# Performance work log

Hardware: AMD Instinct MI355X
Metric: run time of the kernel (lower is better)

## Reference

```python
import jax, jax.numpy as jnp
import numpy as np

B, LQ, LK = 8, 512, 512
DQ = DK = DV = 512
H = 128


def setup_inputs() -> dict:
    key = jax.random.key(0)
    kq, kk, kv, k1, k2, k3 = jax.random.split(key, 6)
    query = jax.random.normal(kq, (B, LQ, DQ), dtype=jnp.float32)
    key_t = jax.random.normal(kk, (B, LK, DK), dtype=jnp.float32)
    value = jax.random.normal(kv, (B, LK, DV), dtype=jnp.float32)
    # Linear weights stored torch-style as (out_features, in_features)
    w1 = jax.random.normal(k1, (H, DQ), dtype=jnp.float32) / np.sqrt(DQ)
    w2 = jax.random.normal(k2, (H, DK), dtype=jnp.float32) / np.sqrt(DK)
    v = jax.random.normal(k3, (1, H), dtype=jnp.float32) / np.sqrt(H)
    return {"query": query, "key": key_t, "value": value, "w1": w1, "w2": w2, "v": v}


def reference(query, key, value, w1, w2, v):
    # Linear projections first (mathematically identical to projecting the
    # broadcast tensors, since Linear is linear): (B,Lq,H), (B,Lk,H)
    q_proj = jnp.einsum("bqd,hd->bqh", query, w1)
    k_proj = jnp.einsum("bkd,hd->bkh", key, w2)
    # Broadcast add -> tanh -> project to scalar: (B,Lq,Lk,H) intermediate
    feat = jnp.tanh(q_proj[:, :, None, :] + k_proj[:, None, :, :])
    score = jnp.einsum("bqkh,h->bqk", feat, v[0])
    attention_weights = jax.nn.softmax(score, axis=-1)
    context_vector = jnp.einsum("bqk,bkv->bqv", attention_weights, value)
    return (attention_weights, context_vector)
```

## Files before the change

kernel.cpp:

```cpp
#include <hip/hip_runtime.h>

#define TWO_LOG2E 2.8853900817779268f

__device__ __forceinline__ float frcp(float x) {
#if __has_builtin(__builtin_amdgcn_rcpf)
  return __builtin_amdgcn_rcpf(x);
#else
  return 1.0f / x;
#endif
}
__device__ __forceinline__ float fexp2(float x) {
#if __has_builtin(__builtin_amdgcn_exp2f)
  return __builtin_amdgcn_exp2f(x);
#else
  return exp2f(x);
#endif
}
__device__ __forceinline__ unsigned short f2bf(float f) {
  unsigned int u = __float_as_uint(f);
  u += 0x7fffu + ((u >> 16) & 1u);
  return (unsigned short)(u >> 16);
}
__device__ __forceinline__ unsigned int pack2bf(float lo, float hi) {
  return (unsigned int)f2bf(lo) | ((unsigned int)f2bf(hi) << 16);
}

using short8 = __attribute__((ext_vector_type(8))) short;
using f32x4v = __attribute__((ext_vector_type(4))) float;
using f32x8s = __attribute__((ext_vector_type(8))) float;
using f32x2 = __attribute__((ext_vector_type(2))) float;

__device__ __forceinline__ f32x2 pkfma(f32x2 a, f32x2 b, f32x2 c) {
  return __builtin_elementwise_fma(a, b, c);
}
__device__ __forceinline__ f32x2 splat2(float x) {
  f32x2 r;
  r.x = x;
  r.y = x;
  return r;
}
__device__ __forceinline__ f32x2 unpack_bf2(unsigned u) {
  f32x2 r;
  r.x = __uint_as_float(u << 16);
  r.y = __uint_as_float(u & 0xffff0000u);
  return r;
}
__device__ __forceinline__ void cell4k(float a0, float a1, float a2, float a3,
                                       f32x2 b0, f32x2 b1, f32x2 b2, f32x2 b3,
                                       float v0, float v1, float v2, float v3,
                                       f32x2& s) {
  const f32x2 one = {1.f, 1.f};
  f32x2 x0 = pkfma(splat2(a0), b0, one);
  f32x2 x1 = pkfma(splat2(a1), b1, one);
  f32x2 x2 = pkfma(splat2(a2), b2, one);
  f32x2 x3 = pkfma(splat2(a3), b3, one);
  f32x2 p01 = x0 * x1, p23 = x2 * x3;
  f32x2 n01 = pkfma(splat2(v0), x1, splat2(v1) * x0);
  f32x2 n23 = pkfma(splat2(v2), x3, splat2(v3) * x2);
  f32x2 num = pkfma(n01, p23, n23 * p01);
  f32x2 den = p01 * p23;
  f32x2 r;
  r.x = frcp(den.x);
  r.y = frcp(den.y);
  s = pkfma(num, r, s);
}

__global__ __launch_bounds__(256) void k_pre(
    const float* __restrict__ query, const float* __restrict__ key,
    const float* __restrict__ w1, const float* __restrict__ w2,
    const float* __restrict__ value,
    float* __restrict__ Aout, unsigned short* __restrict__ BoutT,
    unsigned short* __restrict__ valT) {
  __shared__ __align__(16) char Abuf[16 * 128];
  __shared__ __align__(16) char Bbuf[128 * 128];
  __shared__ unsigned short ts[64][66];

  const int t = threadIdx.x;

  if (blockIdx.y == 0) {
    const int px = blockIdx.x;
    const bool isB = px >= 256;
    const float* in = isB ? key : query;
    const float* wm = isB ? w2 : w1;
    const int m0g = (px & 255) * 16;
    const int w = t >> 6, l = t & 63;

    f32x4v acc[2];
    acc[0] = 0;
    acc[1] = 0;

    float4 aS;
    float4 wS[4][2];

#define P_LOAD(k0_)                                                        \
  {                                                                        \
    aS = *(const float4*)&in[(m0g + (t >> 4)) * 512 + (k0_) + (t & 15) * 4]; \
    _Pragma("unroll") for (int i = 0; i < 4; ++i) {                        \
      int tt = t + i * 256;                                                \
      int row = tt >> 3, g = tt & 7;                                       \
      const float* src = &wm[row * 512 + (k0_) + g * 8];                   \
      wS[i][0] = *(const float4*)src;                                      \
      wS[i][1] = *(const float4*)(src + 4);                                \
    }                                                                      \
  }
#define P_WRITE()                                                          \
  {                                                                        \
    int arow = t >> 4, q4 = t & 15;                                        \
    *(uint2*)(Abuf + arow * 128 + (((q4 >> 1) ^ (arow & 7)) << 4) +        \
              ((q4 & 1) << 3)) =                                           \
        make_uint2(pack2bf(aS.x, aS.y), pack2bf(aS.z, aS.w));              \
    _Pragma("unroll") for (int i = 0; i < 4; ++i) {                        \
      int tt = t + i * 256;                                                \
      int row = tt >> 3, g = tt & 7;                                       \
      uint4 p = make_uint4(                                                \
          pack2bf(wS[i][0].x, wS[i][0].y), pack2bf(wS[i][0].z, wS[i][0].w),\
          pack2bf(wS[i][1].x, wS[i][1].y), pack2bf(wS[i][1].z, wS[i][1].w));\
      *(uint4*)(Bbuf + row * 128 + ((g ^ (row & 7)) << 4)) = p;            \
    }                                                                      \
  }

    P_LOAD(0);
#pragma unroll
    for (int ks8 = 0; ks8 < 8; ++ks8) {
      if (ks8) __syncthreads();
      P_WRITE();
      if (ks8 < 7) P_LOAD(ks8 * 64 + 64);
      __syncthreads();
#pragma unroll
      for (int ks = 0; ks < 2; ++ks) {
        const int gb = ks * 4 + (l >> 4);
        const int ra = l & 15;
        short8 af = *(const short8*)(Abuf + ra * 128 + ((gb ^ (ra & 7)) << 4));
#pragma unroll
        for (int ni = 0; ni < 2; ++ni) {
          const int rb = w * 32 + ni * 16 + (l & 15);
          short8 bf_ = *(const short8*)(Bbuf + rb * 128 + ((gb ^ (rb & 7)) << 4));
          if (isB)
            acc[ni] = __builtin_amdgcn_mfma_f32_16x16x32_bf16(bf_, af, acc[ni], 0, 0, 0);
          else
            acc[ni] = __builtin_amdgcn_mfma_f32_16x16x32_bf16(af, bf_, acc[ni], 0, 0, 0);
        }
      }
    }
#undef P_LOAD
#undef P_WRITE
    if (!isB) {
#pragma unroll
      for (int ni = 0; ni < 2; ++ni) {
        int col = w * 32 + ni * 16 + (l & 15);
#pragma unroll
        for (int j = 0; j < 4; ++j) {
          int row = m0g + (l >> 4) * 4 + j;
          Aout[row * 128 + col] = fexp2(acc[ni][j] * TWO_LOG2E);
        }
      }
    } else {
      int m = m0g + (l & 15);
#pragma unroll
      for (int ni = 0; ni < 2; ++ni)
#pragma unroll
        for (int j = 0; j < 4; ++j) {
          int h = w * 32 + ni * 16 + (l >> 4) * 4 + j;
          BoutT[h * 4096 + m] = f2bf(fexp2(acc[ni][j] * TWO_LOG2E));
        }
    }
  } else {
    const int x = blockIdx.x;
    const int b = x >> 6, k0 = ((x >> 3) & 7) * 64, n0 = (x & 7) * 64;
    {
      int kr = t >> 4, n4 = (t & 15) * 4;
#pragma unroll
      for (int i = 0; i < 4; ++i) {
        float4 f =
            *(const float4*)&value[((b * 512) + k0 + kr + 16 * i) * 512 + n0 + n4];
        *(ushort4*)&ts[kr + 16 * i][n4] =
            make_ushort4(f2bf(f.x), f2bf(f.y), f2bf(f.z), f2bf(f.w));
      }
    }
    __syncthreads();
    {
      int nw = t >> 4, k4 = (t & 15) * 4;
#pragma unroll
      for (int i = 0; i < 4; ++i) {
        int n = nw + 16 * i;
        ushort4 o = make_ushort4(ts[k4 + 0][n], ts[k4 + 1][n], ts[k4 + 2][n],
                                 ts[k4 + 3][n]);
        *(ushort4*)&valT[((b * 512) + n0 + n) * 512 + k0 + k4] = o;
      }
    }
  }
}

__global__ __launch_bounds__(256, 4) void k_score_softmax(
    const float* __restrict__ Aexp, const unsigned short* __restrict__ BexpT,
    const float* __restrict__ vw, float* __restrict__ attn) {
  __shared__ float red[4][4];

  const int tid = threadIdx.x;
  const int b = blockIdx.y;
  const int qbase = blockIdx.x * 4;
  const int wav = tid >> 6;
  const int lane = tid & 63;

  const unsigned* const bbase32 = (const unsigned*)(BexpT + b * 512);
  const int kidx = wav * 64 + lane;

  const float* const pa0 =
      Aexp + __builtin_amdgcn_readfirstlane((b * 512 + qbase) * 128);
  const float* const pa1 = pa0 + 128;
  const float* const pa2 = pa0 + 256;
  const float* const pa3 = pa0 + 384;
  const float* const pv = vw;

  f32x2 acc0 = {0.f, 0.f}, acc1 = {0.f, 0.f};
  f32x2 acc2 = {0.f, 0.f}, acc3 = {0.f, 0.f};

#pragma unroll
  for (int ch = 0; ch < 16; ++ch) {
    f32x8s sa0, sa1, sa2, sa3, sv;
    unsigned soff = (unsigned)(ch * 32);
    asm volatile(
        "s_load_dwordx8 %0, %5, %10\n\t"
        "s_load_dwordx8 %1, %6, %10\n\t"
        "s_load_dwordx8 %2, %7, %10\n\t"
        "s_load_dwordx8 %3, %8, %10\n\t"
        "s_load_dwordx8 %4, %9, %10"
        : "=&s"(sa0), "=&s"(sa1), "=&s"(sa2), "=&s"(sa3), "=&s"(sv)
        : "s"(pa0), "s"(pa1), "s"(pa2), "s"(pa3), "s"(pv), "s"(soff));

    unsigned u[8];
#pragma unroll
    for (int j = 0; j < 8; ++j)
      u[j] = bbase32[ch * 16384 + j * 2048 + kidx];

    asm volatile("s_waitcnt lgkmcnt(0)"
                 : "+s"(sa0), "+s"(sa1), "+s"(sa2), "+s"(sa3), "+s"(sv));

#pragma unroll
    for (int g = 0; g < 2; ++g) {
      f32x2 b0 = unpack_bf2(u[g * 4 + 0]);
      f32x2 b1 = unpack_bf2(u[g * 4 + 1]);
      f32x2 b2 = unpack_bf2(u[g * 4 + 2]);
      f32x2 b3 = unpack_bf2(u[g * 4 + 3]);
      const int h = g * 4;
      cell4k(sa0[h], sa0[h + 1], sa0[h + 2], sa0[h + 3], b0, b1, b2, b3,
             sv[h], sv[h + 1], sv[h + 2], sv[h + 3], acc0);
      cell4k(sa1[h], sa1[h + 1], sa1[h + 2], sa1[h + 3], b0, b1, b2, b3,
             sv[h], sv[h + 1], sv[h + 2], sv[h + 3], acc1);
      cell4k(sa2[h], sa2[h + 1], sa2[h + 2], sa2[h + 3], b0, b1, b2, b3,
             sv[h], sv[h + 1], sv[h + 2], sv[h + 3], acc2);
      cell4k(sa3[h], sa3[h + 1], sa3[h + 2], sa3[h + 3], b0, b1, b2, b3,
             sv[h], sv[h + 1], sv[h + 2], sv[h + 3], acc3);
    }
  }

  float mn0 = fminf(acc0.x, acc0.y);
  float mn1 = fminf(acc1.x, acc1.y);
  float mn2 = fminf(acc2.x, acc2.y);
  float mn3 = fminf(acc3.x, acc3.y);
#pragma unroll
  for (int off = 32; off > 0; off >>= 1) {
    mn0 = fminf(mn0, __shfl_xor(mn0, off));
    mn1 = fminf(mn1, __shfl_xor(mn1, off));
    mn2 = fminf(mn2, __shfl_xor(mn2, off));
    mn3 = fminf(mn3, __shfl_xor(mn3, off));
  }
  if (lane == 0) {
    red[wav][0] = mn0; red[wav][1] = mn1; red[wav][2] = mn2; red[wav][3] = mn3;
  }
  __syncthreads();
  mn0 = fminf(fminf(red[0][0], red[1][0]), fminf(red[2][0], red[3][0]));
  mn1 = fminf(fminf(red[0][1], red[1][1]), fminf(red[2][1], red[3][1]));
  mn2 = fminf(fminf(red[0][2], red[1][2]), fminf(red[2][2], red[3][2]));
  mn3 = fminf(fminf(red[0][3], red[1][3]), fminf(red[2][3], red[3][3]));
  __syncthreads();

  float P0e = fexp2((mn0 - acc0.x) * TWO_LOG2E);
  float P0o = fexp2((mn0 - acc0.y) * TWO_LOG2E);
  float P1e = fexp2((mn1 - acc1.x) * TWO_LOG2E);
  float P1o = fexp2((mn1 - acc1.y) * TWO_LOG2E);
  float P2e = fexp2((mn2 - acc2.x) * TWO_LOG2E);
  float P2o = fexp2((mn2 - acc2.y) * TWO_LOG2E);
  float P3e = fexp2((mn3 - acc3.x) * TWO_LOG2E);
  float P3o = fexp2((mn3 - acc3.y) * TWO_LOG2E);
  float s0 = P0e + P0o, s1 = P1e + P1o, s2 = P2e + P2o, s3 = P3e + P3o;
#pragma unroll
  for (int off = 32; off > 0; off >>= 1) {
    s0 += __shfl_xor(s0, off);
    s1 += __shfl_xor(s1, off);
    s2 += __shfl_xor(s2, off);
    s3 += __shfl_xor(s3, off);
  }
  if (lane == 0) {
    red[wav][0] = s0; red[wav][1] = s1; red[wav][2] = s2; red[wav][3] = s3;
  }
  __syncthreads();
  float r0 = frcp(red[0][0] + red[1][0] + red[2][0] + red[3][0]);
  float r1 = frcp(red[0][1] + red[1][1] + red[2][1] + red[3][1]);
  float r2 = frcp(red[0][2] + red[1][2] + red[2][2] + red[3][2]);
  float r3 = frcp(red[0][3] + red[1][3] + red[2][3] + red[3][3]);

  const int row0 = (b * 512 + qbase) * 512;
  const int k0 = kidx * 2;
  *(float2*)&attn[row0 + k0] = make_float2(P0e * r0, P0o * r0);
  *(float2*)&attn[row0 + 512 + k0] = make_float2(P1e * r1, P1o * r1);
  *(float2*)&attn[row0 + 1024 + k0] = make_float2(P2e * r2, P2o * r2);
  *(float2*)&attn[row0 + 1536 + k0] = make_float2(P3e * r3, P3o * r3);
}

__global__ __launch_bounds__(256) void k_context_mfma(
    const float* __restrict__ attn, const unsigned short* __restrict__ valT,
    float* __restrict__ ctx) {
  __shared__ __align__(16) char At[64 * 128];
  __shared__ __align__(16) char Bt[64 * 128];

  const int t = threadIdx.x;
  const int b = blockIdx.z;
  const int m0 = blockIdx.y * 64, n0 = blockIdx.x * 64;
  const int w = t >> 6, l = t & 63;
  const int wr = w >> 1, wc = w & 1;

  f32x4v acc[2][2];
  acc[0][0] = 0; acc[0][1] = 0; acc[1][0] = 0; acc[1][1] = 0;

  const int sr = t >> 2;
  const int sg = (t & 3);
  const int sswz = sr & 7;

  for (int k0 = 0; k0 < 512; k0 += 64) {
    if (k0) __syncthreads();
    {
      const float* src = &attn[(b * 512 + m0 + sr) * 512 + k0 + sg * 16];
      char* dst = At + sr * 128;
#pragma unroll
      for (int h = 0; h < 2; ++h) {
        float4 f0 = *(const float4*)(src + h * 8);
        float4 f1 = *(const float4*)(src + h * 8 + 4);
        uint4 p = make_uint4(pack2bf(f0.x, f0.y), pack2bf(f0.z, f0.w),
                             pack2bf(f1.x, f1.y), pack2bf(f1.z, f1.w));
        int g = sg * 2 + h;
        *(uint4*)(dst + ((g ^ sswz) << 4)) = p;
      }
      const unsigned short* srcb = &valT[(b * 512 + n0 + sr) * 512 + k0];
      char* dstb = Bt + sr * 128;
#pragma unroll
      for (int h = 0; h < 2; ++h) {
        int g = sg + h * 4;
        uint4 vb = *(const uint4*)(srcb + g * 8);
        *(uint4*)(dstb + ((g ^ sswz) << 4)) = vb;
      }
    }
    __syncthreads();
#pragma unroll
    for (int ks = 0; ks < 2; ++ks) {
      const int gb = ks * 4 + (l >> 4);
      short8 af[2], bf_[2];
#pragma unroll
      for (int mi = 0; mi < 2; ++mi) {
        int ra = wr * 32 + mi * 16 + (l & 15);
        af[mi] = *(const short8*)(At + ra * 128 + ((gb ^ (ra & 7)) << 4));
      }
#pragma unroll
      for (int ni = 0; ni < 2; ++ni) {
        int rb = wc * 32 + ni * 16 + (l & 15);
        bf_[ni] = *(const short8*)(Bt + rb * 128 + ((gb ^ (rb & 7)) << 4));
      }
#pragma unroll
      for (int mi = 0; mi < 2; ++mi)
#pragma unroll
        for (int ni = 0; ni < 2; ++ni)
          acc[mi][ni] = __builtin_amdgcn_mfma_f32_16x16x32_bf16(
              af[mi], bf_[ni], acc[mi][ni], 0, 0, 0);
    }
  }
  __syncthreads();
#pragma unroll
  for (int mi = 0; mi < 2; ++mi)
#pragma unroll
    for (int ni = 0; ni < 2; ++ni) {
      int col = n0 + wc * 32 + ni * 16 + (l & 15);
#pragma unroll
      for (int j = 0; j < 4; ++j) {
        int row = m0 + wr * 32 + mi * 16 + (l >> 4) * 4 + j;
        ctx[(b * 512 + row) * 512 + col] = acc[mi][ni][j];
      }
    }
}

extern "C" void kernel_launch(void* const* d_in, const int* in_sizes, int n_in,
                              void* d_out, int out_size, void* d_ws, size_t ws_size,
                              hipStream_t stream) {
  const float* query = (const float*)d_in[0];
  const float* key   = (const float*)d_in[1];
  const float* value = (const float*)d_in[2];
  const float* w1    = (const float*)d_in[3];
  const float* w2    = (const float*)d_in[4];
  const float* v     = (const float*)d_in[5];

  float* attn = (float*)d_out;
  float* ctx  = attn + 8 * 512 * 512;

  float* Aexp = (float*)d_ws;
  unsigned short* BexpT = (unsigned short*)(Aexp + 4096 * 128);
  unsigned short* valT = BexpT + 128 * 4096;

  k_pre<<<dim3(512, 2), 256, 0, stream>>>(query, key, w1, w2, value,
                                          Aexp, BexpT, valT);
  k_score_softmax<<<dim3(128, 8), 256, 0, stream>>>(Aexp, BexpT, v, attn);
  k_context_mfma<<<dim3(8, 8, 8), 256, 0, stream>>>(attn, valT, ctx);
}
```

Measured before the change: 61.56 us.

## Double-buffer scalar and B loads in score kernel, drop softmax max pass

Restructures the score loop into 32 smaller steps with ping-pong register buffers, so the scalar loads of A and v and the vector loads of B for the next chunk are issued before computing the current one. This hides load latency behind the tanh/FMA work. It also removes the min-reduction pass and its two block barriers before the softmax, exponentiating the accumulator directly. That relies on the score being bounded (sum of |v|·tanh) so exp cannot overflow, and saves one cross-wave reduction.

New measurement: 62.63 us. No clear change (+1.7%).

```diff
diff --git a/kernel.cpp b/kernel.cpp
--- a/kernel.cpp
+++ b/kernel.cpp
@@ -27,7 +27,7 @@
 
 using short8 = __attribute__((ext_vector_type(8))) short;
 using f32x4v = __attribute__((ext_vector_type(4))) float;
-using f32x8s = __attribute__((ext_vector_type(8))) float;
+using f32x4s = __attribute__((ext_vector_type(4))) float;
 using f32x2 = __attribute__((ext_vector_type(2))) float;
 
 __device__ __forceinline__ f32x2 pkfma(f32x2 a, f32x2 b, f32x2 c) {
@@ -207,82 +207,107 @@
 
   const float* const pa0 =
       Aexp + __builtin_amdgcn_readfirstlane((b * 512 + qbase) * 128);
-  const float* const pa1 = pa0 + 128;
-  const float* const pa2 = pa0 + 256;
-  const float* const pa3 = pa0 + 384;
   const float* const pv = vw;
 
   f32x2 acc0 = {0.f, 0.f}, acc1 = {0.f, 0.f};
   f32x2 acc2 = {0.f, 0.f}, acc3 = {0.f, 0.f};
 
-#pragma unroll
-  for (int ch = 0; ch < 16; ++ch) {
-    f32x8s sa0, sa1, sa2, sa3, sv;
-    unsigned soff = (unsigned)(ch * 32);
-    asm volatile(
-        "s_load_dwordx8 %0, %5, %10\n\t"
-        "s_load_dwordx8 %1, %6, %10\n\t"
-        "s_load_dwordx8 %2, %7, %10\n\t"
-        "s_load_dwordx8 %3, %8, %10\n\t"
-        "s_load_dwordx8 %4, %9, %10"
-        : "=&s"(sa0), "=&s"(sa1), "=&s"(sa2), "=&s"(sa3), "=&s"(sv)
-        : "s"(pa0), "s"(pa1), "s"(pa2), "s"(pa3), "s"(pv), "s"(soff));
-
-    unsigned u[8];
-#pragma unroll
-    for (int j = 0; j < 8; ++j)
-      u[j] = bbase32[ch * 16384 + j * 2048 + kidx];
-
-    asm volatile("s_waitcnt lgkmcnt(0)"
-                 : "+s"(sa0), "+s"(sa1), "+s"(sa2), "+s"(sa3), "+s"(sv));
-
-#pragma unroll
-    for (int g = 0; g < 2; ++g) {
-      f32x2 b0 = unpack_bf2(u[g * 4 + 0]);
-      f32x2 b1 = unpack_bf2(u[g * 4 + 1]);
-      f32x2 b2 = unpack_bf2(u[g * 4 + 2]);
-      f32x2 b3 = unpack_bf2(u[g * 4 + 3]);
-      const int h = g * 4;
-      cell4k(sa0[h], sa0[h + 1], sa0[h + 2], sa0[h + 3], b0, b1, b2, b3,
-             sv[h], sv[h + 1], sv[h + 2], sv[h + 3], acc0);
-      cell4k(sa1[h], sa1[h + 1], sa1[h + 2], sa1[h + 3], b0, b1, b2, b3,
-             sv[h], sv[h + 1], sv[h + 2], sv[h + 3], acc1);
-      cell4k(sa2[h], sa2[h + 1], sa2[h + 2], sa2[h + 3], b0, b1, b2, b3,
-             sv[h], sv[h + 1], sv[h + 2], sv[h + 3], acc2);
-      cell4k(sa3[h], sa3[h + 1], sa3[h + 2], sa3[h + 3], b0, b1, b2, b3,
-             sv[h], sv[h + 1], sv[h + 2], sv[h + 3], acc3);
-    }
-  }
-
-  float mn0 = fminf(acc0.x, acc0.y);
-  float mn1 = fminf(acc1.x, acc1.y);
-  float mn2 = fminf(acc2.x, acc2.y);
-  float mn3 = fminf(acc3.x, acc3.y);
-#pragma unroll
-  for (int off = 32; off > 0; off >>= 1) {
-    mn0 = fminf(mn0, __shfl_xor(mn0, off));
-    mn1 = fminf(mn1, __shfl_xor(mn1, off));
-    mn2 = fminf(mn2, __shfl_xor(mn2, off));
-    mn3 = fminf(mn3, __shfl_xor(mn3, off));
-  }
-  if (lane == 0) {
-    red[wav][0] = mn0; red[wav][1] = mn1; red[wav][2] = mn2; red[wav][3] = mn3;
-  }
-  __syncthreads();
-  mn0 = fminf(fminf(red[0][0], red[1][0]), fminf(red[2][0], red[3][0]));
-  mn1 = fminf(fminf(red[0][1], red[1][1]), fminf(red[2][1], red[3][1]));
-  mn2 = fminf(fminf(red[0][2], red[1][2]), fminf(red[2][2], red[3][2]));
-  mn3 = fminf(fminf(red[0][3], red[1][3]), fminf(red[2][3], red[3][3]));
-  __syncthreads();
-
-  float P0e = fexp2((mn0 - acc0.x) * TWO_LOG2E);
-  float P0o = fexp2((mn0 - acc0.y) * TWO_LOG2E);
-  float P1e = fexp2((mn1 - acc1.x) * TWO_LOG2E);
-  float P1o = fexp2((mn1 - acc1.y) * TWO_LOG2E);
-  float P2e = fexp2((mn2 - acc2.x) * TWO_LOG2E);
-  float P2o = fexp2((mn2 - acc2.y) * TWO_LOG2E);
-  float P3e = fexp2((mn3 - acc3.x) * TWO_LOG2E);
-  float P3o = fexp2((mn3 - acc3.y) * TWO_LOG2E);
+  f32x4s A0a, A1a, A2a, A3a, Va, A0b, A1b, A2b, A3b, Vb;
+  unsigned ua[4], ub[4];
+
+#define K2_SMEM(S0_, S1_, S2_, S3_, SV_, COFF_)                            \
+  asm volatile(                                                            \
+      "s_load_dwordx4 %0, %5, %7\n\t"                                      \
+      "s_load_dwordx4 %1, %5, %8\n\t"                                      \
+      "s_load_dwordx4 %2, %5, %9\n\t"                                      \
+      "s_load_dwordx4 %3, %5, %10\n\t"                                     \
+      "s_load_dwordx4 %4, %6, %7"                                          \
+      : "=&s"(S0_), "=&s"(S1_), "=&s"(S2_), "=&s"(S3_), "=&s"(SV_)         \
+      : "s"(pa0), "s"(pv), "i"(COFF_), "i"((COFF_) + 512),                 \
+        "i"((COFF_) + 1024), "i"((COFF_) + 1536))
+
+#define K2_BLD(U_, c_)                                                     \
+  {                                                                        \
+    _Pragma("unroll") for (int j = 0; j < 4; ++j)                          \
+        U_[j] = bbase32[((c_) * 4 + j) * 2048 + kidx];                     \
+  }
+
+#define K2_STEP(c_, S0_, S1_, S2_, S3_, SV_, N0_, N1_, N2_, N3_, NV_,      \
+                UC_, UN_, LAST_)                                           \
+  {                                                                        \
+    asm volatile("s_waitcnt lgkmcnt(0)"                                    \
+                 : "+s"(S0_), "+s"(S1_), "+s"(S2_), "+s"(S3_), "+s"(SV_)); \
+    if (!(LAST_)) {                                                        \
+      K2_SMEM(N0_, N1_, N2_, N3_, NV_, ((c_) + 1) * 16);                   \
+      K2_BLD(UN_, (c_) + 1);                                               \
+    }                                                                      \
+    f32x2 b0 = unpack_bf2(UC_[0]);                                         \
+    f32x2 b1 = unpack_bf2(UC_[1]);                                         \
+    f32x2 b2 = unpack_bf2(UC_[2]);                                         \
+    f32x2 b3 = unpack_bf2(UC_[3]);                                         \
+    cell4k(S0_[0], S0_[1], S0_[2], S0_[3], b0, b1, b2, b3,                 \
+           SV_[0], SV_[1], SV_[2], SV_[3], acc0);                          \
+    cell4k(S1_[0], S1_[1], S1_[2], S1_[3], b0, b1, b2, b3,                 \
+           SV_[0], SV_[1], SV_[2], SV_[3], acc1);                          \
+    cell4k(S2_[0], S2_[1], S2_[2], S2_[3], b0, b1, b2, b3,                 \
+           SV_[0], SV_[1], SV_[2], SV_[3], acc2);                          \
+    cell4k(S3_[0], S3_[1], S3_[2], S3_[3], b0, b1, b2, b3,                 \
+           SV_[0], SV_[1], SV_[2], SV_[3], acc3);                          \
+  }
+
+#define K2_STEP_AB(c_, LAST_)                                              \
+  K2_STEP(c_, A0a, A1a, A2a, A3a, Va, A0b, A1b, A2b, A3b, Vb, ua, ub, LAST_)
+#define K2_STEP_BA(c_, LAST_)                                              \
+  K2_STEP(c_, A0b, A1b, A2b, A3b, Vb, A0a, A1a, A2a, A3a, Va, ub, ua, LAST_)
+
+  K2_SMEM(A0a, A1a, A2a, A3a, Va, 0);
+  K2_BLD(ua, 0);
+  K2_STEP_AB(0, false)
+  K2_STEP_BA(1, false)
+  K2_STEP_AB(2, false)
+  K2_STEP_BA(3, false)
+  K2_STEP_AB(4, false)
+  K2_STEP_BA(5, false)
+  K2_STEP_AB(6, false)
+  K2_STEP_BA(7, false)
+  K2_STEP_AB(8, false)
+  K2_STEP_BA(9, false)
+  K2_STEP_AB(10, false)
+  K2_STEP_BA(11, false)
+  K2_STEP_AB(12, false)
+  K2_STEP_BA(13, false)
+  K2_STEP_AB(14, false)
+  K2_STEP_BA(15, false)
+  K2_STEP_AB(16, false)
+  K2_STEP_BA(17, false)
+  K2_STEP_AB(18, false)
+  K2_STEP_BA(19, false)
+  K2_STEP_AB(20, false)
+  K2_STEP_BA(21, false)
+  K2_STEP_AB(22, false)
+  K2_STEP_BA(23, false)
+  K2_STEP_AB(24, false)
+  K2_STEP_BA(25, false)
+  K2_STEP_AB(26, false)
+  K2_STEP_BA(27, false)
+  K2_STEP_AB(28, false)
+  K2_STEP_BA(29, false)
+  K2_STEP_AB(30, false)
+  K2_STEP_BA(31, true)
+#undef K2_SMEM
+#undef K2_BLD
+#undef K2_STEP
+#undef K2_STEP_AB
+#undef K2_STEP_BA
+
+  float P0e = fexp2(acc0.x * -TWO_LOG2E);
+  float P0o = fexp2(acc0.y * -TWO_LOG2E);
+  float P1e = fexp2(acc1.x * -TWO_LOG2E);
+  float P1o = fexp2(acc1.y * -TWO_LOG2E);
+  float P2e = fexp2(acc2.x * -TWO_LOG2E);
+  float P2o = fexp2(acc2.y * -TWO_LOG2E);
+  float P3e = fexp2(acc3.x * -TWO_LOG2E);
+  float P3o = fexp2(acc3.y * -TWO_LOG2E);
   float s0 = P0e + P0o, s1 = P1e + P1o, s2 = P2e + P2o, s3 = P3e + P3o;
 #pragma unroll
   for (int off = 32; off > 0; off >>= 1) {
```
